# Optimization experiments

Measured on AMD Instinct MI355X. Metric: run time of the kernel, lower is better.

Reference implementation:

```python
import jax, jax.numpy as jnp
import numpy as np

NODE_DIM = 256
HID = 128        # out_channels per head
HEADS = 4
NLAYERS = 2
OUT_DIM = 128
LM, LT = 30, 50
N = LM + LT       # 80 nodes per duplex graph
F = HID * HEADS   # 512
B = 1024
LN_EPS = 1e-5

def _build_edges():
    off = LM
    ms = np.arange(LM - 1); md = ms + 1
    ts = off + np.arange(LT - 1); td = ts + 1
    s1 = np.concatenate([ms, md, ts, td]); d1 = np.concatenate([md, ms, td, ts])
    ms2 = np.arange(LM - 2); md2 = ms2 + 2
    ts2 = off + np.arange(LT - 2); td2 = ts2 + 2
    s2 = np.concatenate([ms2, md2, ts2, td2]); d2 = np.concatenate([md2, ms2, td2, ts2])
    src = np.concatenate([s1, s2]).astype(np.int32)
    dst = np.concatenate([d1, d2]).astype(np.int32)
    etype = np.concatenate([np.zeros(len(s1), np.int32), np.full(len(s2), 2, np.int32)])
    return src, dst, etype

_SRC0, _DST0, _ETYPE0 = _build_edges()
E0 = len(_SRC0)                      # 308 real edges (backbone + proximity)
SRC = jnp.concatenate([jnp.asarray(_SRC0), jnp.arange(N, dtype=jnp.int32)])  # + self loops
DST = jnp.concatenate([jnp.asarray(_DST0), jnp.arange(N, dtype=jnp.int32)])
DST_BASE = jnp.asarray(_DST0)
ETYPE = jnp.asarray(_ETYPE0)

def _ln(x, g, b):
    mu = x.mean(-1, keepdims=True)
    var = ((x - mu) ** 2).mean(-1, keepdims=True)
    return (x - mu) * jax.lax.rsqrt(var + LN_EPS) * g + b

def setup_inputs() -> dict:
    key = jax.random.key(0)
    ks = jax.random.split(key, 24)
    r = lambda k, shape, fan: jax.random.normal(k, shape, jnp.float32) / np.sqrt(fan)
    inp = {
        'mirna_enc': jax.random.normal(ks[0], (B, LM, NODE_DIM), jnp.float32),
        'target_enc': jax.random.normal(ks[1], (B, LT, NODE_DIM), jnp.float32),
        'node_type_emb': r(ks[2], (2, NODE_DIM), NODE_DIM),
        'edge_type_emb': r(ks[3], (3, HEADS), HEADS),
        'in_W': r(ks[4], (NODE_DIM, F), NODE_DIM), 'in_b': jnp.zeros((F,)),
        'in_ln_g': jnp.ones((F,)), 'in_ln_b': jnp.zeros((F,)),
        'gat_Wl': r(ks[5], (NLAYERS, F, F), F), 'gat_bl': jnp.zeros((NLAYERS, F)),
        'gat_Wr': r(ks[6], (NLAYERS, F, F), F), 'gat_br': jnp.zeros((NLAYERS, F)),
        'gat_We': r(ks[7], (NLAYERS, HEADS, F), HEADS),
        'gat_att': r(ks[8], (NLAYERS, HEADS, HID), HID),
        'gat_bo': jnp.zeros((NLAYERS, F)),
        'ln_g': jnp.ones((NLAYERS, F)), 'ln_b': jnp.zeros((NLAYERS, F)),
        'out_W': r(ks[9], (2 * F, OUT_DIM), 2 * F), 'out_b': jnp.zeros((OUT_DIM,)),
        'out_ln_g': jnp.ones((OUT_DIM,)), 'out_ln_b': jnp.zeros((OUT_DIM,)),
    }
    return inp

def reference(mirna_enc, target_enc, node_type_emb, edge_type_emb, in_W, in_b,
              in_ln_g, in_ln_b, gat_Wl, gat_bl, gat_Wr, gat_br, gat_We, gat_att,
              gat_bo, ln_g, ln_b, out_W, out_b, out_ln_g, out_ln_b):
    bsz = mirna_enc.shape[0]
    x = jnp.concatenate([mirna_enc + node_type_emb[0], target_enc + node_type_emb[1]], axis=1)  # [B,N,256]
    x = jax.nn.gelu(_ln(x @ in_W + in_b, in_ln_g, in_ln_b), approximate=False)  # [B,N,F]
    # edge attributes; self-loop attr = per-dst mean of incoming edge attrs (PyG fill_value='mean')
    base = edge_type_emb[ETYPE]  # [E0, HEADS]
    cnt = jax.ops.segment_sum(jnp.ones((E0, 1), base.dtype), DST_BASE, num_segments=N)
    sl = jax.ops.segment_sum(base, DST_BASE, num_segments=N) / jnp.maximum(cnt, 1.0)
    e_attr = jnp.concatenate([base, sl], axis=0)  # [E, HEADS]
    for i in range(NLAYERS):
        ee = (e_attr @ gat_We[i]).reshape(-1, HEADS, HID)                 # [E,H,C]
        xl = (x @ gat_Wl[i] + gat_bl[i]).reshape(bsz, N, HEADS, HID)
        xr = (x @ gat_Wr[i] + gat_br[i]).reshape(bsz, N, HEADS, HID)
        att_i = gat_att[i]
        def one_graph(xl_b, xr_b):
            msg = xl_b[SRC] + xr_b[DST] + ee                              # [E,H,C]
            a = jnp.einsum('ehc,hc->eh', jax.nn.leaky_relu(msg, 0.2), att_i)
            amax = jax.ops.segment_max(a, DST, num_segments=N)            # every node has a self loop
            ex = jnp.exp(a - amax[DST])
            den = jax.ops.segment_sum(ex, DST, num_segments=N)
            alpha = ex / den[DST]                                         # [E,H]
            out = jax.ops.segment_sum(alpha[:, :, None] * xl_b[SRC], DST, num_segments=N)
            return out.reshape(N, F)
        h = jax.vmap(one_graph)(xl, xr) + gat_bo[i]
        x = _ln(h + x, ln_g[i], ln_b[i])
        if i < NLAYERS - 1:
            x = jax.nn.gelu(x, approximate=False)
    pooled = jnp.concatenate([x.mean(axis=1), x.max(axis=1)], axis=-1)    # [B, 2F]
    return jax.nn.gelu(_ln(pooled @ out_W + out_b, out_ln_g, out_ln_b), approximate=False)
```

## Files before the change

kernel.cpp:

```cpp
#include <hip/hip_runtime.h>
#include <hip/hip_bf16.h>

typedef unsigned short u16;
typedef unsigned int u32;
typedef __attribute__((ext_vector_type(8))) short bf16x8;
typedef __attribute__((ext_vector_type(4))) float f32x4;

#define NB   1024
#define LMI  30
#define LTG  50
#define NN   80
#define ROWS (NB*NN)
#define FF   512
#define HH   4
#define CC   128

__device__ __forceinline__ u16 f2b(float f) {
    u32 u = __float_as_uint(f);
    u32 r = (u + 0x7FFFu + ((u >> 16) & 1u)) >> 16;
    return (u16)r;
}
__device__ __forceinline__ float b2f(u16 h) {
    return __uint_as_float(((u32)h) << 16);
}
__device__ __forceinline__ float gelu_f(float v) {
    return 0.5f * v * (1.0f + erff(v * 0.70710678118654752440f));
}
__device__ __forceinline__ void gload_lds16(const void* g, void* l) {
    __builtin_amdgcn_global_load_lds(
        (__attribute__((address_space(1))) void*)(uintptr_t)g,
        (__attribute__((address_space(3))) void*)(uintptr_t)l,
        16, 0, 0);
}

#define X_OFF     0ULL
#define XLR_OFF   83886080ULL
#define INWT_OFF  251658240ULL
#define WLRT_OFF  (INWT_OFF + 262144ULL)
#define BIAS_OFF  (WLRT_OFF + 2097152ULL)
#define EER_OFF   (BIAS_OFF + 8192ULL)
#define EES_OFF   (EER_OFF + 8192ULL)

__global__ __launch_bounds__(256)
void prep_misc(const float* __restrict__ in_W, const float* __restrict__ gat_Wl,
               const float* __restrict__ gat_bl, const float* __restrict__ gat_Wr,
               const float* __restrict__ gat_br, const float* __restrict__ gat_We,
               const float* __restrict__ eemb,
               u16* __restrict__ inWt, u16* __restrict__ Wlrt,
               float* __restrict__ biaslr, float* __restrict__ eereal,
               float* __restrict__ eeself)
{
    int idx = blockIdx.x * 256 + threadIdx.x;
    if (idx < 131072) {
        int n = idx >> 8, k = idx & 255;
        inWt[idx] = f2b(in_W[k * 512 + n]);
        return;
    }
    idx -= 131072;
    if (idx < 1048576) {
        int l = idx >> 19; int r = idx & 524287; int n = r >> 9, k = r & 511;
        float v = (n < 512) ? gat_Wl[(size_t)l * 262144 + (size_t)k * 512 + n]
                            : gat_Wr[(size_t)l * 262144 + (size_t)k * 512 + (n - 512)];
        Wlrt[idx] = f2b(v);
        return;
    }
    idx -= 1048576;
    if (idx < 2048) {
        int l = idx >> 10, n = idx & 1023;
        biaslr[idx] = (n < 512) ? gat_bl[l * 512 + n] : gat_br[l * 512 + (n - 512)];
        return;
    }
    idx -= 2048;
    if (idx < 2048) {
        int l = idx >> 10; int r = idx & 1023; int t = r >> 9, f = r & 511;
        int et = t ? 2 : 0;
        float v = 0.f;
        #pragma unroll
        for (int h = 0; h < 4; ++h)
            v += eemb[et * 4 + h] * gat_We[l * 2048 + h * 512 + f];
        eereal[idx] = v;
        return;
    }
    idx -= 2048;
    if (idx < 81920) {
        int l = idx / 40960; int r = idx % 40960; int n = r >> 9, f = r & 511;
        int LL = (n < LMI) ? LMI : LTG;
        int p  = (n < LMI) ? n : (n - LMI);
        float c1 = (float)((p >= 1) + (p <= LL - 2));
        float c2 = (float)((p >= 2) + (p <= LL - 3));
        float ic = 1.0f / (c1 + c2);
        float v = 0.f;
        #pragma unroll
        for (int h = 0; h < 4; ++h) {
            float attr = (c1 * eemb[0 * 4 + h] + c2 * eemb[2 * 4 + h]) * ic;
            v += attr * gat_We[l * 2048 + h * 512 + f];
        }
        eeself[idx] = v;
        return;
    }
}

__global__ __launch_bounds__(64)
void prep_xin(const float* __restrict__ mirna, const float* __restrict__ target,
              const float* __restrict__ nte, u16* __restrict__ xin)
{
    int bid = blockIdx.x;
    int b = bid / NN, n = bid % NN;
    int t = threadIdx.x;
    const float* src; const float* tv;
    if (n < LMI) { src = mirna + ((size_t)b * LMI + n) * 256; tv = nte; }
    else         { src = target + ((size_t)b * LTG + (n - LMI)) * 256; tv = nte + 256; }
    float4 v = *(const float4*)(src + t * 4);
    float4 e = *(const float4*)(tv + t * 4);
    u32 p0 = (u32)f2b(v.x + e.x) | ((u32)f2b(v.y + e.y) << 16);
    u32 p1 = (u32)f2b(v.z + e.z) | ((u32)f2b(v.w + e.w) << 16);
    *(uint2*)(xin + (size_t)bid * 256 + t * 4) = make_uint2(p0, p1);
}

__global__ __launch_bounds__(256, 2)
void gemm_nt_bias(const u16* __restrict__ A, const u16* __restrict__ Bt,
                  const float* __restrict__ bias, u16* __restrict__ Cout,
                  int N, int K)
{
    __shared__ __align__(16) u16 Asm[128 * 32];
    __shared__ __align__(16) u16 Bsm[128 * 32];
    const int tid = threadIdx.x;
    const int w = tid >> 6, l = tid & 63;
    const int row0 = blockIdx.y * 128;
    const int col0 = blockIdx.x * 128;
    const int wr = (w & 1) * 64, wc = (w >> 1) * 64;

    const int c0 = 2 * w, c1 = 2 * w + 1;
    const int lrow = l >> 2;
    const int lcol = (l & 3) * 8;
    const u16* Ag0 = A  + (size_t)(row0 + c0 * 16 + lrow) * K + lcol;
    const u16* Ag1 = A  + (size_t)(row0 + c1 * 16 + lrow) * K + lcol;
    const u16* Bg0 = Bt + (size_t)(col0 + c0 * 16 + lrow) * K + lcol;
    const u16* Bg1 = Bt + (size_t)(col0 + c1 * 16 + lrow) * K + lcol;
    u16* Al0 = &Asm[c0 * 512];
    u16* Al1 = &Asm[c1 * 512];
    u16* Bl0 = &Bsm[c0 * 512];
    u16* Bl1 = &Bsm[c1 * 512];

    const f32x4 vzero = {0.f, 0.f, 0.f, 0.f};
    f32x4 acc[4][4];
    #pragma unroll
    for (int r = 0; r < 4; ++r)
        #pragma unroll
        for (int f = 0; f < 4; ++f) acc[r][f] = vzero;

    const int nsteps = K >> 5;
    for (int ks = 0; ks < nsteps; ++ks) {
        int ko = ks << 5;
        __syncthreads();
        gload_lds16(Ag0 + ko, Al0);
        gload_lds16(Ag1 + ko, Al1);
        gload_lds16(Bg0 + ko, Bl0);
        gload_lds16(Bg1 + ko, Bl1);
        __syncthreads();
        bf16x8 af[4], bfr[4];
        #pragma unroll
        for (int r = 0; r < 4; ++r)
            af[r] = *(const bf16x8*)&Asm[(wr + r * 16 + (l & 15)) * 32 + (l >> 4) * 8];
        #pragma unroll
        for (int f = 0; f < 4; ++f)
            bfr[f] = *(const bf16x8*)&Bsm[(wc + f * 16 + (l & 15)) * 32 + (l >> 4) * 8];
        #pragma unroll
        for (int r = 0; r < 4; ++r)
            #pragma unroll
            for (int f = 0; f < 4; ++f)
                acc[r][f] = __builtin_amdgcn_mfma_f32_16x16x32_bf16(af[r], bfr[f], acc[r][f], 0, 0, 0);
    }

    #pragma unroll
    for (int r = 0; r < 4; ++r) {
        int grow = row0 + wr + r * 16 + (l >> 4) * 4;
        #pragma unroll
        for (int f = 0; f < 4; ++f) {
            int gcol = col0 + wc + f * 16 + (l & 15);
            float bv = bias[gcol];
            #pragma unroll
            for (int j = 0; j < 4; ++j) {
                float v = acc[r][f][j] + bv;
                Cout[(size_t)(grow + j) * N + gcol] = f2b(v);
            }
        }
    }
}

__global__ __launch_bounds__(256)
void ln_gelu_rows(u16* __restrict__ x, const float* __restrict__ g, const float* __restrict__ b)
{
    int w = threadIdx.x >> 6, l = threadIdx.x & 63;
    size_t row = (size_t)blockIdx.x * 4 + w;
    u16* rp = x + row * FF + l * 8;
    bf16x8 v = *(const bf16x8*)rp;
    float y[8]; float s = 0.f, q = 0.f;
    #pragma unroll
    for (int j = 0; j < 8; ++j) { y[j] = b2f((u16)v[j]); s += y[j]; q += y[j] * y[j]; }
    #pragma unroll
    for (int st = 32; st; st >>= 1) { s += __shfl_xor(s, st, 64); q += __shfl_xor(q, st, 64); }
    float mu = s * (1.0f / 512.0f);
    float var = q * (1.0f / 512.0f) - mu * mu;
    float rs = rsqrtf(var + 1e-5f);
    float4 g0 = *(const float4*)(g + l * 8), g1 = *(const float4*)(g + l * 8 + 4);
    float4 b0 = *(const float4*)(b + l * 8), b1 = *(const float4*)(b + l * 8 + 4);
    float gv[8] = {g0.x, g0.y, g0.z, g0.w, g1.x, g1.y, g1.z, g1.w};
    float bv[8] = {b0.x, b0.y, b0.z, b0.w, b1.x, b1.y, b1.z, b1.w};
    bf16x8 o;
    #pragma unroll
    for (int j = 0; j < 8; ++j) {
        float z = (y[j] - mu) * rs * gv[j] + bv[j];
        o[j] = (short)f2b(gelu_f(z));
    }
    *(bf16x8*)rp = o;
}

__global__ __launch_bounds__(256)
void gat_layer(u16* __restrict__ x, const u16* __restrict__ xlr,
               const float* __restrict__ att, const float* __restrict__ eereal,
               const float* __restrict__ eeself, const float* __restrict__ bo,
               const float* __restrict__ g, const float* __restrict__ bta,
               int apply_gelu)
{
    int tid = threadIdx.x;
    int h = tid >> 6, l = tid & 63;
    int s = l >> 4, t = l & 15;
    int row = blockIdx.x * 4 + s;
    int n = row % NN;
    int lo = (n < LMI) ? 0 : LMI;
    int hi = (n < LMI) ? (LMI - 1) : (NN - 1);
    int c = h * CC + t * 8;

    bf16x8 xrv = *(const bf16x8*)(xlr + (size_t)row * 1024 + 512 + c);
    float xr[8], atv[8];
    #pragma unroll
    for (int j = 0; j < 8; ++j) xr[j] = b2f((u16)xrv[j]);
    {
        float4 a0 = *(const float4*)(att + c), a1 = *(const float4*)(att + c + 4);
        atv[0]=a0.x; atv[1]=a0.y; atv[2]=a0.z; atv[3]=a0.w;
        atv[4]=a1.x; atv[5]=a1.y; atv[6]=a1.z; atv[7]=a1.w;
    }

    bf16x8 vsave[5];
    float p5[5];
    float amax = -1e30f;
    #pragma unroll
    for (int i = 0; i < 5; ++i) {
        int d = i - 2;
        int src = n + d;
        bool ok = (src >= lo) && (src <= hi);
        int dd = ok ? d : 0;
        bf16x8 vv = *(const bf16x8*)(xlr + (size_t)(row + dd) * 1024 + c);
        vsave[i] = vv;
        const float* ee = (i == 2) ? (eeself + (size_t)n * 512 + c)
                        : ((i == 1 || i == 3) ? (eereal + c) : (eereal + 512 + c));
        float4 e0 = *(const float4*)ee, e1 = *(const float4*)(ee + 4);
        float eez[8] = {e0.x, e0.y, e0.z, e0.w, e1.x, e1.y, e1.z, e1.w};
        float p = 0.f;
        #pragma unroll
        for (int j = 0; j < 8; ++j) {
            float m = b2f((u16)vv[j]) + xr[j] + eez[j];
            m = m > 0.f ? m : 0.2f * m;
            p += m * atv[j];
        }
        p += __shfl_xor(p, 1, 64);
        p += __shfl_xor(p, 2, 64);
        p += __shfl_xor(p, 4, 64);
        p += __shfl_xor(p, 8, 64);
        p = ok ? p : -1e30f;
        p5[i] = p;
        amax = fmaxf(amax, p);
    }
    float den = 0.f;
    float o[8] = {0.f,0.f,0.f,0.f,0.f,0.f,0.f,0.f};
    #pragma unroll
    for (int i = 0; i < 5; ++i) {
        float ex = __expf(p5[i] - amax);
        den += ex;
        #pragma unroll
        for (int j = 0; j < 8; ++j) o[j] += ex * b2f((u16)vsave[i][j]);
    }
    float inv = 1.0f / den;

    u16* xrow = x + (size_t)row * FF + c;
    bf16x8 xv = *(const bf16x8*)xrow;
    float bov[8];
    {
        float4 b0 = *(const float4*)(bo + c), b1 = *(const float4*)(bo + c + 4);
        bov[0]=b0.x; bov[1]=b0.y; bov[2]=b0.z; bov[3]=b0.w;
        bov[4]=b1.x; bov[5]=b1.y; bov[6]=b1.z; bov[7]=b1.w;
    }
    float y[8]; float sum = 0.f, sq = 0.f;
    #pragma unroll
    for (int j = 0; j < 8; ++j) {
        y[j] = o[j] * inv + bov[j] + b2f((u16)xv[j]);
        sum += y[j]; sq += y[j] * y[j];
    }
    sum += __shfl_xor(sum, 1, 64); sq += __shfl_xor(sq, 1, 64);
    sum += __shfl_xor(sum, 2, 64); sq += __shfl_xor(sq, 2, 64);
    sum += __shfl_xor(sum, 4, 64); sq += __shfl_xor(sq, 4, 64);
    sum += __shfl_xor(sum, 8, 64); sq += __shfl_xor(sq, 8, 64);

    __shared__ float ssum[4][4], ssq[4][4];
    if (t == 0) { ssum[h][s] = sum; ssq[h][s] = sq; }
    __syncthreads();
    float tot = ssum[0][s] + ssum[1][s] + ssum[2][s] + ssum[3][s];
    float tq  = ssq[0][s] + ssq[1][s] + ssq[2][s] + ssq[3][s];
    float mu = tot * (1.0f / 512.0f);
    float var = tq * (1.0f / 512.0f) - mu * mu;
    float rs = rsqrtf(var + 1e-5f);

    float gv[8], btv[8];
    {
        float4 g0 = *(const float4*)(g + c), g1 = *(const float4*)(g + c + 4);
        float4 t0 = *(const float4*)(bta + c), t1 = *(const float4*)(bta + c + 4);
        gv[0]=g0.x; gv[1]=g0.y; gv[2]=g0.z; gv[3]=g0.w;
        gv[4]=g1.x; gv[5]=g1.y; gv[6]=g1.z; gv[7]=g1.w;
        btv[0]=t0.x; btv[1]=t0.y; btv[2]=t0.z; btv[3]=t0.w;
        btv[4]=t1.x; btv[5]=t1.y; btv[6]=t1.z; btv[7]=t1.w;
    }
    bf16x8 ov;
    #pragma unroll
    for (int j = 0; j < 8; ++j) {
        float z = (y[j] - mu) * rs * gv[j] + btv[j];
        if (apply_gelu) z = gelu_f(z);
        ov[j] = (short)f2b(z);
    }
    *(bf16x8*)xrow = ov;
}

__global__ __launch_bounds__(512)
void pool_kernel(const u16* __restrict__ x, u16* __restrict__ pooled)
{
    int b = blockIdx.x;
    int f = threadIdx.x;
    const u16* base = x + (size_t)b * NN * FF + f;
    float s = 0.f, mx = -1e30f;
    #pragma unroll 4
    for (int n = 0; n < NN; ++n) {
        float v = b2f(base[(size_t)n * FF]);
        s += v; mx = fmaxf(mx, v);
    }
    pooled[(size_t)b * 1024 + f]       = f2b(s * (1.0f / 80.0f));
    pooled[(size_t)b * 1024 + 512 + f] = f2b(mx);
}

__global__ __launch_bounds__(128)
void out_head(const u16* __restrict__ pooled, const float* __restrict__ W,
              const float* __restrict__ bia, const float* __restrict__ g,
              const float* __restrict__ bt, float* __restrict__ out)
{
    int b = blockIdx.x;
    int j = threadIdx.x;
    __shared__ float prow[1024];
    for (int i = j; i < 1024; i += 128) prow[i] = b2f(pooled[(size_t)b * 1024 + i]);
    __syncthreads();
    float acc = 0.f;
    #pragma unroll 8
    for (int k = 0; k < 1024; ++k) acc += prow[k] * W[k * 128 + j];
    acc += bia[j];
    float s = acc, q = acc * acc;
    #pragma unroll
    for (int st = 32; st; st >>= 1) { s += __shfl_xor(s, st, 64); q += __shfl_xor(q, st, 64); }
    __shared__ float ps[2], pq[2];
    int w = j >> 6;
    if ((j & 63) == 0) { ps[w] = s; pq[w] = q; }
    __syncthreads();
    float tot = ps[0] + ps[1], tq = pq[0] + pq[1];
    float mu = tot * (1.0f / 128.0f);
    float var = tq * (1.0f / 128.0f) - mu * mu;
    float rs = rsqrtf(var + 1e-5f);
    float z = (acc - mu) * rs * g[j] + bt[j];
    out[(size_t)b * 128 + j] = gelu_f(z);
}

extern "C" void kernel_launch(void* const* d_in, const int* in_sizes, int n_in,
                              void* d_out, int out_size, void* d_ws, size_t ws_size,
                              hipStream_t stream)
{
    (void)in_sizes; (void)n_in; (void)out_size; (void)ws_size;
    const float* mirna    = (const float*)d_in[0];
    const float* target   = (const float*)d_in[1];
    const float* nte      = (const float*)d_in[2];
    const float* eemb     = (const float*)d_in[3];
    const float* in_W     = (const float*)d_in[4];
    const float* in_b     = (const float*)d_in[5];
    const float* in_ln_g  = (const float*)d_in[6];
    const float* in_ln_b  = (const float*)d_in[7];
    const float* gat_Wl   = (const float*)d_in[8];
    const float* gat_bl   = (const float*)d_in[9];
    const float* gat_Wr   = (const float*)d_in[10];
    const float* gat_br   = (const float*)d_in[11];
    const float* gat_We   = (const float*)d_in[12];
    const float* gat_att  = (const float*)d_in[13];
    const float* gat_bo   = (const float*)d_in[14];
    const float* ln_g     = (const float*)d_in[15];
    const float* ln_b     = (const float*)d_in[16];
    const float* out_W    = (const float*)d_in[17];
    const float* out_b    = (const float*)d_in[18];
    const float* out_ln_g = (const float*)d_in[19];
    const float* out_ln_b = (const float*)d_in[20];

    char* ws = (char*)d_ws;
    u16*   x      = (u16*)(ws + X_OFF);
    u16*   xlr    = (u16*)(ws + XLR_OFF);
    u16*   xin    = xlr;
    u16*   pooled = xlr;
    u16*   inWt   = (u16*)(ws + INWT_OFF);
    u16*   Wlrt   = (u16*)(ws + WLRT_OFF);
    float* biaslr = (float*)(ws + BIAS_OFF);
    float* eereal = (float*)(ws + EER_OFF);
    float* eeself = (float*)(ws + EES_OFF);

    prep_misc<<<4944, 256, 0, stream>>>(in_W, gat_Wl, gat_bl, gat_Wr, gat_br, gat_We, eemb,
                                        inWt, Wlrt, biaslr, eereal, eeself);
    prep_xin<<<ROWS, 64, 0, stream>>>(mirna, target, nte, xin);

    dim3 g1(512 / 128, ROWS / 128);
    gemm_nt_bias<<<g1, 256, 0, stream>>>(xin, inWt, in_b, x, 512, 256);
    ln_gelu_rows<<<ROWS / 4, 256, 0, stream>>>(x, in_ln_g, in_ln_b);

    for (int l = 0; l < 2; ++l) {
        dim3 g2(1024 / 128, ROWS / 128);
        gemm_nt_bias<<<g2, 256, 0, stream>>>(x, Wlrt + (size_t)l * 524288,
                                             biaslr + l * 1024, xlr, 1024, 512);
        gat_layer<<<ROWS / 4, 256, 0, stream>>>(x, xlr,
                                                gat_att + l * 512,
                                                eereal + l * 1024,
                                                eeself + (size_t)l * 40960,
                                                gat_bo + l * 512,
                                                ln_g + l * 512, ln_b + l * 512,
                                                (l == 0) ? 1 : 0);
    }

    pool_kernel<<<NB, 512, 0, stream>>>(x, pooled);
    out_head<<<NB, 128, 0, stream>>>(pooled, out_W, out_b, out_ln_g, out_ln_b, (float*)d_out);
}
```

Baseline: 619.0 us.

## Double-buffer GEMM LDS loads, swizzle blocks per XCD, vectorize epilogue stores

Rewrites the bf16 MFMA GEMM main loop to keep two LDS stages in flight, using explicit vmcnt waits and barriers so global-to-LDS loads for step t+2 overlap compute on step t. It moves to a 1D grid remapped so that consecutive tiles land on the same XCD, which should improve L2 reuse. It also changes the LDS layout to k-major chunks and swaps the MFMA operand order, so each lane writes four contiguous bf16 outputs with one 8-byte store plus a float4 bias load. The risks are correctness of the manual waitcnt accounting and a doubled LDS footprint that may lower occupancy.

```diff
diff --git a/kernel.cpp b/kernel.cpp
--- a/kernel.cpp
+++ b/kernel.cpp
@@ -120,27 +120,37 @@
 __global__ __launch_bounds__(256, 2)
 void gemm_nt_bias(const u16* __restrict__ A, const u16* __restrict__ Bt,
                   const float* __restrict__ bias, u16* __restrict__ Cout,
-                  int N, int K)
-{
-    __shared__ __align__(16) u16 Asm[128 * 32];
-    __shared__ __align__(16) u16 Bsm[128 * 32];
+                  int N, int K, int ncb)
+{
+    __shared__ __align__(16) u16 sm[2][2][4096];
     const int tid = threadIdx.x;
     const int w = tid >> 6, l = tid & 63;
-    const int row0 = blockIdx.y * 128;
-    const int col0 = blockIdx.x * 128;
+
+    int nwg = gridDim.x;
+    int per = nwg >> 3;
+    int xcd = blockIdx.x & 7, sub = blockIdx.x >> 3;
+    int nid = xcd * per + sub;
+    const int row0 = (nid / ncb) * 128;
+    const int col0 = (nid % ncb) * 128;
     const int wr = (w & 1) * 64, wc = (w >> 1) * 64;
 
-    const int c0 = 2 * w, c1 = 2 * w + 1;
-    const int lrow = l >> 2;
-    const int lcol = (l & 3) * 8;
-    const u16* Ag0 = A  + (size_t)(row0 + c0 * 16 + lrow) * K + lcol;
-    const u16* Ag1 = A  + (size_t)(row0 + c1 * 16 + lrow) * K + lcol;
-    const u16* Bg0 = Bt + (size_t)(col0 + c0 * 16 + lrow) * K + lcol;
-    const u16* Bg1 = Bt + (size_t)(col0 + c1 * 16 + lrow) * K + lcol;
-    u16* Al0 = &Asm[c0 * 512];
-    u16* Al1 = &Asm[c1 * 512];
-    u16* Bl0 = &Bsm[c0 * 512];
-    u16* Bl1 = &Bsm[c1 * 512];
+    const u16* Ag = A  + (size_t)(row0 + l) * K + w * 8;
+    const u16* Bg = Bt + (size_t)(col0 + l) * K + w * 8;
+    const size_t rstep = (size_t)64 * K;
+    u16* AL0 = &sm[0][0][w * 1024];
+    u16* AL1 = &sm[1][0][w * 1024];
+    u16* BL0 = &sm[0][1][w * 1024];
+    u16* BL1 = &sm[1][1][w * 1024];
+
+#define STAGE(b, t) do {                                    \
+        int _ko = (t) << 5;                                 \
+        u16* _al = (b) ? AL1 : AL0;                         \
+        u16* _bl = (b) ? BL1 : BL0;                         \
+        gload_lds16(Ag + _ko,         _al);                 \
+        gload_lds16(Ag + rstep + _ko, _al + 512);           \
+        gload_lds16(Bg + _ko,         _bl);                 \
+        gload_lds16(Bg + rstep + _ko, _bl + 512);           \
+    } while (0)
 
     const f32x4 vzero = {0.f, 0.f, 0.f, 0.f};
     f32x4 acc[4][4];
@@ -150,40 +160,49 @@
         for (int f = 0; f < 4; ++f) acc[r][f] = vzero;
 
     const int nsteps = K >> 5;
-    for (int ks = 0; ks < nsteps; ++ks) {
-        int ko = ks << 5;
-        __syncthreads();
-        gload_lds16(Ag0 + ko, Al0);
-        gload_lds16(Ag1 + ko, Al1);
-        gload_lds16(Bg0 + ko, Bl0);
-        gload_lds16(Bg1 + ko, Bl1);
-        __syncthreads();
+    STAGE(0, 0);
+    STAGE(1, 1);
+
+    const int aoff = (l >> 4) * 1024 + (l & 15) * 8;
+    for (int t = 0; t < nsteps; ++t) {
+        int b = t & 1;
+        if (t < nsteps - 1) {
+            asm volatile("s_waitcnt vmcnt(4)" ::: "memory");
+        } else {
+            asm volatile("s_waitcnt vmcnt(0)" ::: "memory");
+        }
+        __builtin_amdgcn_s_barrier();
+        asm volatile("" ::: "memory");
+
         bf16x8 af[4], bfr[4];
         #pragma unroll
         for (int r = 0; r < 4; ++r)
-            af[r] = *(const bf16x8*)&Asm[(wr + r * 16 + (l & 15)) * 32 + (l >> 4) * 8];
+            af[r] = *(const bf16x8*)&sm[b][0][aoff + (wr + r * 16) * 8];
         #pragma unroll
         for (int f = 0; f < 4; ++f)
-            bfr[f] = *(const bf16x8*)&Bsm[(wc + f * 16 + (l & 15)) * 32 + (l >> 4) * 8];
+            bfr[f] = *(const bf16x8*)&sm[b][1][aoff + (wc + f * 16) * 8];
         #pragma unroll
         for (int r = 0; r < 4; ++r)
             #pragma unroll
             for (int f = 0; f < 4; ++f)
-                acc[r][f] = __builtin_amdgcn_mfma_f32_16x16x32_bf16(af[r], bfr[f], acc[r][f], 0, 0, 0);
-    }
+                acc[r][f] = __builtin_amdgcn_mfma_f32_16x16x32_bf16(bfr[f], af[r], acc[r][f], 0, 0, 0);
+
+        asm volatile("" ::: "memory");
+        __builtin_amdgcn_s_barrier();
+        if (t + 2 < nsteps) STAGE(b, t + 2);
+    }
+#undef STAGE
 
     #pragma unroll
     for (int r = 0; r < 4; ++r) {
-        int grow = row0 + wr + r * 16 + (l >> 4) * 4;
+        int grow = row0 + wr + r * 16 + (l & 15);
         #pragma unroll
         for (int f = 0; f < 4; ++f) {
-            int gcol = col0 + wc + f * 16 + (l & 15);
-            float bv = bias[gcol];
-            #pragma unroll
-            for (int j = 0; j < 4; ++j) {
-                float v = acc[r][f][j] + bv;
-                Cout[(size_t)(grow + j) * N + gcol] = f2b(v);
-            }
+            int n0 = col0 + wc + f * 16 + (l >> 4) * 4;
+            float4 bv = *(const float4*)(bias + n0);
+            u32 lo = (u32)f2b(acc[r][f][0] + bv.x) | ((u32)f2b(acc[r][f][1] + bv.y) << 16);
+            u32 hi = (u32)f2b(acc[r][f][2] + bv.z) | ((u32)f2b(acc[r][f][3] + bv.w) << 16);
+            *(uint2*)&Cout[(size_t)grow * N + n0] = make_uint2(lo, hi);
         }
     }
 }
@@ -417,14 +436,12 @@
                                         inWt, Wlrt, biaslr, eereal, eeself);
     prep_xin<<<ROWS, 64, 0, stream>>>(mirna, target, nte, xin);
 
-    dim3 g1(512 / 128, ROWS / 128);
-    gemm_nt_bias<<<g1, 256, 0, stream>>>(xin, inWt, in_b, x, 512, 256);
+    gemm_nt_bias<<<(ROWS / 128) * 4, 256, 0, stream>>>(xin, inWt, in_b, x, 512, 256, 4);
     ln_gelu_rows<<<ROWS / 4, 256, 0, stream>>>(x, in_ln_g, in_ln_b);
 
     for (int l = 0; l < 2; ++l) {
-        dim3 g2(1024 / 128, ROWS / 128);
-        gemm_nt_bias<<<g2, 256, 0, stream>>>(x, Wlrt + (size_t)l * 524288,
-                                             biaslr + l * 1024, xlr, 1024, 512);
+        gemm_nt_bias<<<(ROWS / 128) * 8, 256, 0, stream>>>(x, Wlrt + (size_t)l * 524288,
+                                                           biaslr + l * 1024, xlr, 1024, 512, 8);
         gat_layer<<<ROWS / 4, 256, 0, stream>>>(x, xlr,
                                                 gat_att + l * 512,
                                                 eereal + l * 1024,
```

Result: slower. 725.8 us (+17.3%).
